# Kernel tuning notes

Hardware: AMD Instinct MI355X
Metric: run time of the kernel (lower is better)

Reference implementation:

```python
import jax, jax.numpy as jnp
import numpy as np

B, C, HID, A, K = 128, 2, 150, 8, 30
GRID = 49           # input maze size (forward crops to 49x49)
HP = GRID + 2       # 51: spatial size after kernel=3, padding=2 convs
KS = 3              # value-iteration kernel size


def conv(x, w, b=None, pad=1):
    y = jax.lax.conv_general_dilated(
        x, w, (1, 1), [(pad, pad), (pad, pad)],
        dimension_numbers=('NCHW', 'OIHW', 'NCHW'))
    if b is not None:
        y = y + b[None, :, None, None]
    return y


def unfold9(v):
    # v: [B,1,HP,HP] -> [B,9,HP,HP], 3x3 patches, padding=1 (matches F.unfold)
    vp = jnp.pad(v[:, 0], ((0, 0), (1, 1), (1, 1)))
    return jnp.stack([vp[:, i:i + HP, j:j + HP]
                      for i in range(KS) for j in range(KS)], axis=1)


def setup_inputs() -> dict:
    key = jax.random.key(0)
    ks = jax.random.split(key, 13)
    s = 0.05
    return {
        'grid': (jax.random.uniform(ks[0], (B, C, GRID, GRID)) < 0.3).astype(jnp.float32),
        'x_coord': jax.random.randint(ks[1], (B,), 0, GRID - 2),
        'y_coord': jax.random.randint(ks[2], (B,), 0, GRID - 2),
        'h1_w': jax.random.normal(ks[3], (HID, C, 3, 3)) * s,
        'h1_b': jax.random.normal(ks[4], (HID,)) * s,
        'h2_w': jax.random.normal(ks[5], (HID, HID, 3, 3)) * s,
        'h2_b': jax.random.normal(ks[6], (HID,)) * s,
        'r_w': jax.random.normal(ks[7], (1, HID, 3, 3)) * s,
        't_w': jax.random.normal(ks[8], (A * KS * KS, HID, 3, 3)) * s,
        'a1_w': jax.random.normal(ks[9], (HID, A)) * s,
        'a1_b': jax.random.normal(ks[10], (HID,)) * s,
        'a2_w': jax.random.normal(ks[11], (A, HID)) * s,
        'a2_b': jax.random.normal(ks[12], (A,)) * s,
    }


def reference(grid, x_coord, y_coord, h1_w, h1_b, h2_w, h2_b, r_w, t_w,
              a1_w, a1_b, a2_w, a2_b):
    # hidden feature extractor (padding=1, keeps 49x49)
    h = jax.nn.relu(conv(grid, h1_w, h1_b, pad=1))
    h = jax.nn.relu(conv(h, h2_w, h2_b, pad=1))
    # reward & dynamic transitions (kernel=3, padding=2 -> 51x51)
    reward = conv(h, r_w, None, pad=2)                 # [B,1,51,51]
    trans = conv(h, t_w, None, pad=2)                  # [B,A*9,51,51]
    # softmax over the 9-element kernel dim (loop-invariant in the original)
    sT = jax.nn.softmax(trans.reshape(B, A, KS * KS, HP, HP), axis=2)

    def step(carry, _):
        v, _ = carry
        patches = unfold9(v)                           # [B,9,51,51]
        q = jnp.einsum('bakhw,bkhw->bahw', sT, patches) + reward
        v_new = jnp.max(q, axis=1, keepdims=True)      # [B,1,51,51]
        return (v_new, q), None

    q0 = jnp.zeros((B, A, HP, HP), grid.dtype)
    (v, q_last), _ = jax.lax.scan(step, (jnp.zeros_like(reward), q0),
                                  None, length=K)

    # per-pixel action MLP on cropped q from the LAST iteration
    q_c = q_last[:, :, :GRID, :GRID]                   # [B,A,49,49]
    mid = jax.nn.relu(jnp.einsum('bahw,ca->bchw', q_c, a1_w)
                      + a1_b[None, :, None, None])
    logits = (jnp.einsum('bchw,ac->bahw', mid, a2_w)
              + a2_b[None, :, None, None])             # [B,A,49,49]
    return logits
```

## Files before the change

kernel.cpp:

```cpp
#include <hip/hip_runtime.h>
#include <hip/hip_bf16.h>
#include <stdint.h>

constexpr int NB   = 128;
constexpr int NC   = 2;
constexpr int NH   = 150;
constexpr int NA   = 8;
constexpr int KIT  = 30;
constexpr int GN   = 49;
constexpr int HPN  = 51;
constexpr int NP   = HPN * HPN;
constexpr int RTC  = 73;
constexpr int CIP  = 160;

typedef short v8bf __attribute__((ext_vector_type(8)));
typedef float v4f  __attribute__((ext_vector_type(4)));

__device__ __forceinline__ float bf_lo(uint32_t u){ return __uint_as_float(u << 16); }
__device__ __forceinline__ float bf_hi(uint32_t u){ return __uint_as_float(u & 0xffff0000u); }

__device__ __forceinline__ uint16_t f2bf(float f) {
    uint32_t u = __float_as_uint(f);
    uint32_t lsb = (u >> 16) & 1u;
    u += 0x7fffu + lsb;
    return (uint16_t)(u >> 16);
}

__device__ __forceinline__ float ld_f(const void* p, size_t i, int isbf) {
    if (isbf) {
        uint32_t b = ((const uint16_t*)p)[i];
        return __uint_as_float(b << 16);
    }
    return ((const float*)p)[i];
}
__device__ __forceinline__ uint16_t ld_bf_bits(const void* p, size_t i, int isbf) {
    if (isbf) return ((const uint16_t*)p)[i];
    return f2bf(((const float*)p)[i]);
}

__global__ void detect_kernel(const uint16_t* __restrict__ w, int* __restrict__ flag)
{
    int i = threadIdx.x;
    uint32_t bits = w[2 * i];
    float f = __uint_as_float(bits << 16);
    float a = fabsf(f);
    bool ok = (a >= 1e-10f && a <= 1e5f);
    unsigned long long m = __ballot(ok);
    if (i == 0) flag[0] = (__popcll(m) >= 48) ? 1 : 0;
}

__global__ void prep_kernel(const void* __restrict__ g,
                            const void* __restrict__ w1,
                            const void* __restrict__ b1,
                            const void* __restrict__ w2,
                            const void* __restrict__ b2,
                            const void* __restrict__ rw,
                            const void* __restrict__ tw,
                            const void* __restrict__ a1w,
                            const void* __restrict__ a1b,
                            const void* __restrict__ a2w,
                            const void* __restrict__ a2b,
                            const int* __restrict__ flag,
                            uint16_t* __restrict__ grid_cl,
                            float* __restrict__ wT1, float* __restrict__ bias1,
                            uint16_t* __restrict__ w2t, float* __restrict__ bias2,
                            uint16_t* __restrict__ wrt,
                            float* __restrict__ wA1, float* __restrict__ bA1,
                            float* __restrict__ wA2, float* __restrict__ bA2)
{
    constexpr int N_GRID = NB * GN * GN * NC;
    constexpr int N_WT1  = 9 * NC * NH;
    constexpr int N_B1   = NH;
    constexpr int N_W2T  = 9 * 5 * CIP * 32;
    constexpr int N_B2   = CIP;
    constexpr int N_WRT  = 9 * 5 * 80 * 32;
    constexpr int N_A1W  = NH * NA;
    constexpr int N_A1B  = NH;
    constexpr int N_A2W  = NA * NH;
    constexpr int N_A2B  = NA;

    int isbf = flag[0];
    int i = blockIdx.x * blockDim.x + threadIdx.x;
    if (i < N_GRID) {
        int c = i & 1; int s = (i >> 1) % (GN*GN); int b = i / (GN*GN*2);
        grid_cl[i] = ld_bf_bits(g, (size_t)(b*NC + c)*(GN*GN) + s, isbf);
        return;
    }
    i -= N_GRID;
    if (i < N_WT1) {
        int co = i % NH; int r = i / NH; int ci = r & 1; int k = r >> 1;
        wT1[i] = ld_f(w1, (size_t)co*(NC*9) + ci*9 + k, isbf);
        return;
    }
    i -= N_WT1;
    if (i < N_B1) { bias1[i] = ld_f(b1, i, isbf); return; }
    i -= N_B1;
    if (i < N_W2T) {
        int c  = i % 32;
        int co = (i / 32) % CIP;
        int kc = (i / (32*CIP)) % 5;
        int tap = i / (32*CIP*5);
        int ci = kc*32 + c;
        uint16_t v = 0;
        if (co < NH && ci < NH)
            v = f2bf(ld_f(w2, ((size_t)co*NH + ci)*9 + tap, isbf));
        w2t[i] = v;
        return;
    }
    i -= N_W2T;
    if (i < N_B2) { bias2[i] = (i < NH) ? ld_f(b2, i, isbf) : 0.f; return; }
    i -= N_B2;
    if (i < N_WRT) {
        int c  = i % 32;
        int co = (i / 32) % 80;
        int kc = (i / 2560) % 5;
        int tap = i / 12800;
        int ci = kc*32 + c;
        uint16_t v = 0;
        if (ci < NH) {
            if (co == 0)        v = f2bf(ld_f(rw, (size_t)ci*9 + tap, isbf));
            else if (co <= 72)  v = f2bf(ld_f(tw, ((size_t)(co-1)*NH + ci)*9 + tap, isbf));
        }
        wrt[i] = v;
        return;
    }
    i -= N_WRT;
    if (i < N_A1W) { wA1[i] = ld_f(a1w, i, isbf); return; }
    i -= N_A1W;
    if (i < N_A1B) { bA1[i] = ld_f(a1b, i, isbf); return; }
    i -= N_A1B;
    if (i < N_A2W) { wA2[i] = ld_f(a2w, i, isbf); return; }
    i -= N_A2W;
    if (i < N_A2B) { bA2[i] = ld_f(a2b, i, isbf); return; }
}

__global__ __launch_bounds__(192)
void conv1_cl(const uint16_t* __restrict__ in,
              const float* __restrict__ wT,
              const float* __restrict__ bias,
              uint16_t* __restrict__ out)
{
    constexpr int H = GN, XG = 13;
    int bid = blockIdx.x;
    int xg = bid % XG;
    int y  = (bid / XG) % H;
    int b  = bid / (XG * H);
    int x0 = xg * 4;
    int co = threadIdx.x;

    if (co >= NH) {
        if (co < CIP) {
            #pragma unroll
            for (int xi = 0; xi < 4; ++xi) {
                int x = x0 + xi;
                if (x < H) out[((size_t)(b*H + y)*H + x)*CIP + co] = 0;
            }
        }
        return;
    }

    float bv = bias[co];
    float acc[4] = {bv, bv, bv, bv};

    for (int ky = 0; ky < 3; ++ky) {
        int yy = y + ky - 1;
        if (yy < 0 || yy >= H) continue;
        const uint16_t* rowp = in + (size_t)(b * H + yy) * H * NC;
        #pragma unroll
        for (int kx = 0; kx < 3; ++kx) {
            const float* wp = wT + ((ky*3 + kx) * NC) * NH + co;
            float w0 = wp[0];
            float w1 = wp[NH];
            #pragma unroll
            for (int xi = 0; xi < 4; ++xi) {
                int xx = x0 + xi + kx - 1;
                if (xx < 0 || xx >= H) continue;
                uint32_t u = *(const uint32_t*)(rowp + (size_t)xx * NC);
                acc[xi] += bf_lo(u)*w0 + bf_hi(u)*w1;
            }
        }
    }
    #pragma unroll
    for (int xi = 0; xi < 4; ++xi) {
        int x = x0 + xi;
        if (x < H) out[((size_t)(b*H + y)*H + x)*CIP + co] = f2bf(fmaxf(acc[xi], 0.f));
    }
}

template<int CO_T, int CO_S, int PAD, int OH, bool RELU, bool OBF>
__global__ __launch_bounds__(192)
void conv_mfma(const uint16_t* __restrict__ in,
               const uint16_t* __restrict__ wt,
               const float* __restrict__ bias,
               void* __restrict__ outv)
{
    constexpr int H = GN;
    constexpr int NSUB = CO_S / 16;
    constexpr int CS = CO_T / CO_S;
    constexpr int AS = 168;
    constexpr int NST = 45;
    static_assert(NSUB * 16 == CO_S && CS * CO_S == CO_T, "");

    __shared__ __align__(16) uint16_t shA[8 * 18 * AS];

    int bid = blockIdx.x;
    int cs = 0;
    if (CS > 1) { cs = bid % CS; bid /= CS; }
    int xg = bid & 3;
    int rg = (bid >> 2) % 9;
    int b  = bid / 36;
    int y0 = rg * 6, x0 = xg * 16;
    int co0 = cs * CO_S;
    int t = threadIdx.x;
    int w = t >> 6, l = t & 63;
    int lo16 = l & 15, q4 = l >> 4;

    for (int q = t; q < 8*18*20; q += 192) {
        int ci8 = q % 20;
        int c   = (q / 20) % 18;
        int r   = q / 360;
        int yy = y0 + r - PAD, xx = x0 + c - PAD;
        uint4 v = make_uint4(0u, 0u, 0u, 0u);
        if (yy >= 0 && yy < H && xx >= 0 && xx < H)
            v = *(const uint4*)(in + ((size_t)(b*H + yy)*H + xx)*CIP + ci8*8);
        *(uint4*)(&shA[(r*18 + c)*AS + ci8*8]) = v;
    }
    __syncthreads();

    const uint16_t* wbase = wt + (size_t)co0*32 + lo16*32 + q4*8;

    v4f acc[2][NSUB];
    #pragma unroll
    for (int si = 0; si < 2; ++si)
        #pragma unroll
        for (int n = 0; n < NSUB; ++n)
            acc[si][n] = (v4f){0.f, 0.f, 0.f, 0.f};

    auto loadB = [&](int s, v8bf* bf) {
        const uint16_t* p = wbase + (size_t)s * (CO_T*32);
        #pragma unroll
        for (int n = 0; n < NSUB; ++n)
            bf[n] = *(const v8bf*)(p + n*512);
    };
    auto loadA = [&](int s, v8bf* af) {
        int tap = s / 5, kc = s % 5;
        int ky = tap / 3, kx = tap % 3;
        const uint16_t* base = &shA[((2*w + ky)*18 + lo16 + kx)*AS + kc*32 + q4*8];
        af[0] = *(const v8bf*)(base);
        af[1] = *(const v8bf*)(base + 18*AS);
    };
    auto compute = [&](v8bf* af, v8bf* bf) {
        #pragma unroll
        for (int n = 0; n < NSUB; ++n) {
            acc[0][n] = __builtin_amdgcn_mfma_f32_16x16x32_bf16(af[0], bf[n], acc[0][n], 0, 0, 0);
            acc[1][n] = __builtin_amdgcn_mfma_f32_16x16x32_bf16(af[1], bf[n], acc[1][n], 0, 0, 0);
        }
    };

    v8bf bf0[NSUB], bf1[NSUB], af0[2], af1[2];
    loadB(0, bf0); loadA(0, af0);
    for (int s = 0; s < NST - 1; s += 2) {
        loadB(s + 1, bf1); loadA(s + 1, af1);
        compute(af0, bf0);
        if (s + 2 < NST) { loadB(s + 2, bf0); loadA(s + 2, af0); }
        compute(af1, bf1);
    }
    compute(af0, bf0);

    #pragma unroll
    for (int si = 0; si < 2; ++si) {
        int y = y0 + 2*w + si;
        if (y >= OH) continue;
        #pragma unroll
        for (int n = 0; n < NSUB; ++n) {
            int co = co0 + n*16 + lo16;
            float bv = bias ? bias[co] : 0.f;
            #pragma unroll
            for (int r = 0; r < 4; ++r) {
                int x = x0 + q4*4 + r;
                if (x >= OH) continue;
                float v = acc[si][n][r] + bv;
                if (RELU) v = fmaxf(v, 0.f);
                if (OBF) {
                    ((uint16_t*)outv)[((size_t)(b*OH + y)*OH + x)*CIP + co] = f2bf(v);
                } else {
                    if (co < RTC)
                        ((float*)outv)[((size_t)(b*OH + y)*OH + x)*RTC + co] = v;
                }
            }
        }
    }
}

__global__ void softmax_pack_kernel(const float* __restrict__ rt,
                                    uint32_t* __restrict__ sTu,
                                    float* __restrict__ rewb)
{
    int idx = blockIdx.x * blockDim.x + threadIdx.x;
    constexpr int TOT = NB * NP;
    if (idx >= TOT) return;
    const float* tp = rt + (size_t)idx * RTC;
    rewb[idx] = tp[0];
    uint32_t words[36];
    #pragma unroll
    for (int a = 0; a < NA; ++a) {
        const float* s = tp + 1 + a * 9;
        float v[9];
        float m = -1e30f;
        #pragma unroll
        for (int k = 0; k < 9; ++k) { v[k] = s[k]; m = fmaxf(m, v[k]); }
        float sum = 0.f;
        #pragma unroll
        for (int k = 0; k < 9; ++k) { v[k] = expf(v[k] - m); sum += v[k]; }
        float sc = 65535.f / sum;
        #pragma unroll
        for (int k = 0; k < 9; ++k) {
            int gi = a * 9 + k;
            uint32_t u = (uint32_t)__float2uint_rn(v[k] * sc);
            if (gi & 1) words[gi >> 1] |= (u << 16);
            else        words[gi >> 1] = u;
        }
    }
    uint32_t* op = sTu + (size_t)idx * 36;
    #pragma unroll
    for (int j = 0; j < 9; ++j)
        *(uint4*)(op + 4*j) = make_uint4(words[4*j], words[4*j+1], words[4*j+2], words[4*j+3]);
}

__device__ __forceinline__ void vi_pair(const uint32_t* d, const float* pat,
                                        float r, float& qE, float& qO)
{
    float qe = 0.f, qo = 0.f;
    qe = fmaf((float)(d[0] & 0xffffu), pat[0], qe);
    qe = fmaf((float)(d[0] >> 16),     pat[1], qe);
    qe = fmaf((float)(d[1] & 0xffffu), pat[2], qe);
    qe = fmaf((float)(d[1] >> 16),     pat[3], qe);
    qe = fmaf((float)(d[2] & 0xffffu), pat[4], qe);
    qe = fmaf((float)(d[2] >> 16),     pat[5], qe);
    qe = fmaf((float)(d[3] & 0xffffu), pat[6], qe);
    qe = fmaf((float)(d[3] >> 16),     pat[7], qe);
    qe = fmaf((float)(d[4] & 0xffffu), pat[8], qe);
    qo = fmaf((float)(d[4] >> 16),     pat[0], qo);
    qo = fmaf((float)(d[5] & 0xffffu), pat[1], qo);
    qo = fmaf((float)(d[5] >> 16),     pat[2], qo);
    qo = fmaf((float)(d[6] & 0xffffu), pat[3], qo);
    qo = fmaf((float)(d[6] >> 16),     pat[4], qo);
    qo = fmaf((float)(d[7] & 0xffffu), pat[5], qo);
    qo = fmaf((float)(d[7] >> 16),     pat[6], qo);
    qo = fmaf((float)(d[8] & 0xffffu), pat[7], qo);
    qo = fmaf((float)(d[8] >> 16),     pat[8], qo);
    constexpr float inv = 1.f / 65535.f;
    qE = fmaf(qe, inv, r);
    qO = fmaf(qo, inv, r);
}

__global__ __launch_bounds__(1024, 1)
void vi_kernel(const uint32_t* __restrict__ sTu, const float* __restrict__ rewb,
               float* __restrict__ qout)
{
    __shared__ float vb[2][53*53];
    __shared__ float rew[NP];
    int b = blockIdx.x, t = threadIdx.x;
    for (int i = t; i < 53*53; i += 1024) { vb[0][i] = 0.f; vb[1][i] = 0.f; }
    const uint32_t* sb = sTu + (size_t)b * NP * 36;
    for (int i = t; i < NP; i += 1024) rew[i] = rewb[(size_t)b * NP + i];

    int p0 = t, p1 = t + 1024, p2 = t + 2048;
    uint32_t s0[36], s1[36];
    {
        const uint4* a0 = (const uint4*)(sb + (size_t)p0 * 36);
        const uint4* a1 = (const uint4*)(sb + (size_t)p1 * 36);
        #pragma unroll
        for (int j = 0; j < 9; ++j) {
            uint4 v = a0[j];
            s0[4*j+0]=v.x; s0[4*j+1]=v.y; s0[4*j+2]=v.z; s0[4*j+3]=v.w;
            uint4 u = a1[j];
            s1[4*j+0]=u.x; s1[4*j+1]=u.y; s1[4*j+2]=u.z; s1[4*j+3]=u.w;
        }
    }
    __syncthreads();

    float* qb = qout + (size_t)b * NP * NA;
    int cur = 0;
    for (int it = 0; it < KIT; ++it) {
        bool last = (it == KIT - 1);
        const float* vc = vb[cur];
        float* vn = vb[cur ^ 1];
        {
            int y = p0 / HPN, x = p0 % HPN;
            float pat[9];
            #pragma unroll
            for (int dy = 0; dy < 3; ++dy)
                #pragma unroll
                for (int dx = 0; dx < 3; ++dx)
                    pat[dy*3+dx] = vc[(y+dy)*53 + x+dx];
            float r = rew[p0];
            float best = -3.4e38f;
            #pragma unroll
            for (int ap = 0; ap < 4; ++ap) {
                float qE, qO;
                vi_pair(s0 + ap*9, pat, r, qE, qO);
                best = fmaxf(best, fmaxf(qE, qO));
                if (last) {
                    qb[(size_t)p0*NA + 2*ap]     = qE;
                    qb[(size_t)p0*NA + 2*ap + 1] = qO;
                }
            }
            vn[(y+1)*53 + x+1] = best;
        }
        {
            int y = p1 / HPN, x = p1 % HPN;
            float pat[9];
            #pragma unroll
            for (int dy = 0; dy < 3; ++dy)
                #pragma unroll
                for (int dx = 0; dx < 3; ++dx)
                    pat[dy*3+dx] = vc[(y+dy)*53 + x+dx];
            float r = rew[p1];
            float best = -3.4e38f;
            #pragma unroll
            for (int ap = 0; ap < 4; ++ap) {
                float qE, qO;
                vi_pair(s1 + ap*9, pat, r, qE, qO);
                best = fmaxf(best, fmaxf(qE, qO));
                if (last) {
                    qb[(size_t)p1*NA + 2*ap]     = qE;
                    qb[(size_t)p1*NA + 2*ap + 1] = qO;
                }
            }
            vn[(y+1)*53 + x+1] = best;
        }
        if (t < NP - 2048) {
            int y = p2 / HPN, x = p2 % HPN;
            float pat[9];
            #pragma unroll
            for (int dy = 0; dy < 3; ++dy)
                #pragma unroll
                for (int dx = 0; dx < 3; ++dx)
                    pat[dy*3+dx] = vc[(y+dy)*53 + x+dx];
            float r = rew[p2];
            float best = -3.4e38f;
            const uint32_t* gp = sb + (size_t)p2 * 36;
            #pragma unroll
            for (int ap = 0; ap < 4; ++ap) {
                uint32_t d[9];
                #pragma unroll
                for (int j = 0; j < 9; ++j) d[j] = gp[ap*9 + j];
                float qE, qO;
                vi_pair(d, pat, r, qE, qO);
                best = fmaxf(best, fmaxf(qE, qO));
                if (last) {
                    qb[(size_t)p2*NA + 2*ap]     = qE;
                    qb[(size_t)p2*NA + 2*ap + 1] = qO;
                }
            }
            vn[(y+1)*53 + x+1] = best;
        }
        __syncthreads();
        cur ^= 1;
    }
}

__global__ void head_kernel(const float* __restrict__ q,
                            const float* __restrict__ wA1,
                            const float* __restrict__ bA1,
                            const float* __restrict__ wA2,
                            const float* __restrict__ bA2,
                            const int* __restrict__ flag,
                            void* __restrict__ out)
{
    __shared__ float w1[NH*NA], sb1[NH], w2[NA*NH], sb2[NA];
    int t = threadIdx.x;
    for (int i = t; i < NH*NA; i += 256) w1[i] = wA1[i];
    for (int i = t; i < NH;    i += 256) sb1[i] = bA1[i];
    for (int i = t; i < NA*NH; i += 256) w2[i] = wA2[i];
    if (t < NA) sb2[t] = bA2[t];
    __syncthreads();

    int isbf = flag[0];
    int idx = blockIdx.x * 256 + t;
    constexpr int TOT = NB * GN * GN;
    if (idx >= TOT) return;
    int x = idx % GN, y = (idx / GN) % GN, b = idx / (GN*GN);
    const float* qp = q + ((size_t)(b*HPN + y)*HPN + x) * NA;
    float qv[NA];
    #pragma unroll
    for (int a = 0; a < NA; ++a) qv[a] = qp[a];
    float lg[NA];
    #pragma unroll
    for (int a = 0; a < NA; ++a) lg[a] = sb2[a];
    for (int c = 0; c < NH; ++c) {
        float m = sb1[c];
        #pragma unroll
        for (int a = 0; a < NA; ++a) m += qv[a] * w1[c*NA + a];
        m = fmaxf(m, 0.f);
        #pragma unroll
        for (int a = 0; a < NA; ++a) lg[a] += m * w2[a*NH + c];
    }
    #pragma unroll
    for (int a = 0; a < NA; ++a) {
        size_t oi = ((size_t)(b*NA + a)*GN + y)*GN + x;
        float r = lg[a];
        if (isbf) ((uint16_t*)out)[oi] = f2bf(r);
        else      ((float*)out)[oi] = r;
    }
}

extern "C" void kernel_launch(void* const* d_in, const int* in_sizes, int n_in,
                              void* d_out, int out_size, void* d_ws, size_t ws_size,
                              hipStream_t stream)
{
    const void* g   = d_in[0];
    const void* h1w = d_in[3];
    const void* h1b = d_in[4];
    const void* h2w = d_in[5];
    const void* h2b = d_in[6];
    const void* rw  = d_in[7];
    const void* tw  = d_in[8];
    const void* a1w = d_in[9];
    const void* a1b = d_in[10];
    const void* a2w = d_in[11];
    const void* a2b = d_in[12];

    char* ws = (char*)d_ws;
    size_t off = 0;
    auto take = [&](size_t bytes) { size_t r = off; off = (off + bytes + 255) & ~(size_t)255; return r; };

    constexpr size_t N_GRID_CL = (size_t)NB*GN*GN*NC;
    constexpr size_t N_WT1  = 9*NC*NH;
    constexpr size_t N_B1   = NH;
    constexpr size_t N_W2T  = 9*5*CIP*32;
    constexpr size_t N_B2   = CIP;
    constexpr size_t N_WRT  = 9*5*80*32;
    constexpr size_t N_A1W  = NH*NA;
    constexpr size_t N_A1B  = NH;
    constexpr size_t N_A2W  = NA*NH;
    constexpr size_t N_A2B  = NA;
    constexpr size_t N_H    = (size_t)NB*GN*GN*CIP;
    constexpr size_t N_RT   = (size_t)NB*NP*RTC;
    constexpr size_t N_Q    = (size_t)NB*NP*NA;
    constexpr size_t N_STU  = (size_t)NB*NP*36;
    constexpr size_t N_REWB = (size_t)NB*NP;

    size_t off_flag   = take(4);
    size_t off_gridcl = take(N_GRID_CL * 2);
    size_t off_wT1    = take(N_WT1 * 4);
    size_t off_b1     = take(N_B1 * 4);
    size_t off_w2t    = take(N_W2T * 2);
    size_t off_b2     = take(N_B2 * 4);
    size_t off_wrt    = take(N_WRT * 2);
    size_t off_wA1    = take(N_A1W * 4);
    size_t off_bA1    = take(N_A1B * 4);
    size_t off_wA2    = take(N_A2W * 4);
    size_t off_bA2    = take(N_A2B * 4);
    size_t off_q      = take(N_Q * 4);
    size_t szA = (N_RT * 4 > N_H * 2) ? N_RT * 4 : N_H * 2;
    size_t off_A      = take(szA);
    size_t szB = N_H * 2;
    size_t szB2 = ((N_STU * 4 + 255) & ~(size_t)255) + N_REWB * 4;
    if (szB2 > szB) szB = szB2;
    size_t off_B      = take(szB);

    int*      flag    = (int*)(ws + off_flag);
    uint16_t* grid_cl = (uint16_t*)(ws + off_gridcl);
    float*    wT1     = (float*)(ws + off_wT1);
    float*    bias1   = (float*)(ws + off_b1);
    uint16_t* w2t     = (uint16_t*)(ws + off_w2t);
    float*    bias2   = (float*)(ws + off_b2);
    uint16_t* wrt     = (uint16_t*)(ws + off_wrt);
    float*    wA1     = (float*)(ws + off_wA1);
    float*    bA1     = (float*)(ws + off_bA1);
    float*    wA2     = (float*)(ws + off_wA2);
    float*    bA2     = (float*)(ws + off_bA2);
    float*    qbuf    = (float*)(ws + off_q);
    uint16_t* h1      = (uint16_t*)(ws + off_A);
    float*    rt      = (float*)(ws + off_A);
    uint16_t* h2      = (uint16_t*)(ws + off_B);
    uint32_t* sTu     = (uint32_t*)(ws + off_B);
    float*    rewb    = (float*)(ws + off_B + ((N_STU * 4 + 255) & ~(size_t)255));

    detect_kernel<<<1, 64, 0, stream>>>((const uint16_t*)h2w, flag);
    {
        int total = (int)(N_GRID_CL + N_WT1 + N_B1 + N_W2T + N_B2 + N_WRT
                          + N_A1W + N_A1B + N_A2W + N_A2B);
        prep_kernel<<<(total + 255)/256, 256, 0, stream>>>(
            g, h1w, h1b, h2w, h2b, rw, tw, a1w, a1b, a2w, a2b, flag,
            grid_cl, wT1, bias1, w2t, bias2, wrt, wA1, bA1, wA2, bA2);
    }
    conv1_cl<<<NB*GN*13, 192, 0, stream>>>(grid_cl, wT1, bias1, h1);
    conv_mfma<CIP, 80, 1, GN, true, true>
        <<<NB*36*2, 192, 0, stream>>>(h1, w2t, bias2, (void*)h2);
    conv_mfma<80, 80, 2, HPN, false, false>
        <<<NB*36, 192, 0, stream>>>(h2, wrt, nullptr, (void*)rt);
    softmax_pack_kernel<<<(NB*NP + 255)/256, 256, 0, stream>>>(rt, sTu, rewb);
    vi_kernel<<<NB, 1024, 0, stream>>>(sTu, rewb, qbuf);
    head_kernel<<<(NB*GN*GN + 255)/256, 256, 0, stream>>>(qbuf, wA1, bA1, wA2, bA2, flag,
                                                          d_out);
}
```

Baseline: 1.281 ms.

## Split conv halo staging into two channel phases to shrink LDS footprint

The MFMA conv kernel now stages the input halo in two channel chunks (3 then 2 of the 5 k-chunks), computing each phase before reloading shared memory. This cuts LDS per block from 168 to 104 stride, which should allow more resident blocks per CU. The cost is extra barriers, a serialized second global load without overlap, and shorter MFMA pipelines per phase.

```diff
diff --git a/kernel.cpp b/kernel.cpp
--- a/kernel.cpp
+++ b/kernel.cpp
@@ -197,11 +197,10 @@
     constexpr int H = GN;
     constexpr int NSUB = CO_S / 16;
     constexpr int CS = CO_T / CO_S;
-    constexpr int AS = 168;
-    constexpr int NST = 45;
+    constexpr int ASP = 104;
     static_assert(NSUB * 16 == CO_S && CS * CO_S == CO_T, "");
 
-    __shared__ __align__(16) uint16_t shA[8 * 18 * AS];
+    __shared__ __align__(16) uint16_t shA[8 * 18 * ASP];
 
     int bid = blockIdx.x;
     int cs = 0;
@@ -215,17 +214,20 @@
     int w = t >> 6, l = t & 63;
     int lo16 = l & 15, q4 = l >> 4;
 
-    for (int q = t; q < 8*18*20; q += 192) {
-        int ci8 = q % 20;
-        int c   = (q / 20) % 18;
-        int r   = q / 360;
-        int yy = y0 + r - PAD, xx = x0 + c - PAD;
-        uint4 v = make_uint4(0u, 0u, 0u, 0u);
-        if (yy >= 0 && yy < H && xx >= 0 && xx < H)
-            v = *(const uint4*)(in + ((size_t)(b*H + yy)*H + xx)*CIP + ci8*8);
-        *(uint4*)(&shA[(r*18 + c)*AS + ci8*8]) = v;
-    }
-    __syncthreads();
+    auto stageHalo = [&](int kcBase, int nkc) {
+        int nch = nkc * 4;
+        int total = 8 * 18 * nch;
+        for (int q = t; q < total; q += 192) {
+            int ci8 = q % nch;
+            int c   = (q / nch) % 18;
+            int r   = q / (nch * 18);
+            int yy = y0 + r - PAD, xx = x0 + c - PAD;
+            uint4 v = make_uint4(0u, 0u, 0u, 0u);
+            if (yy >= 0 && yy < H && xx >= 0 && xx < H)
+                v = *(const uint4*)(in + ((size_t)(b*H + yy)*H + xx)*CIP + kcBase*32 + ci8*8);
+            *(uint4*)(&shA[(r*18 + c)*ASP + ci8*8]) = v;
+        }
+    };
 
     const uint16_t* wbase = wt + (size_t)co0*32 + lo16*32 + q4*8;
 
@@ -236,18 +238,18 @@
         for (int n = 0; n < NSUB; ++n)
             acc[si][n] = (v4f){0.f, 0.f, 0.f, 0.f};
 
-    auto loadB = [&](int s, v8bf* bf) {
-        const uint16_t* p = wbase + (size_t)s * (CO_T*32);
+    auto loadB = [&](int sg, v8bf* bf) {
+        const uint16_t* p = wbase + (size_t)sg * (CO_T*32);
         #pragma unroll
         for (int n = 0; n < NSUB; ++n)
             bf[n] = *(const v8bf*)(p + n*512);
     };
-    auto loadA = [&](int s, v8bf* af) {
-        int tap = s / 5, kc = s % 5;
+    auto loadA = [&](int sg, int kcBase, v8bf* af) {
+        int tap = sg / 5, kc = sg % 5;
         int ky = tap / 3, kx = tap % 3;
-        const uint16_t* base = &shA[((2*w + ky)*18 + lo16 + kx)*AS + kc*32 + q4*8];
+        const uint16_t* base = &shA[((2*w + ky)*18 + lo16 + kx)*ASP + (kc - kcBase)*32 + q4*8];
         af[0] = *(const v8bf*)(base);
-        af[1] = *(const v8bf*)(base + 18*AS);
+        af[1] = *(const v8bf*)(base + 18*ASP);
     };
     auto compute = [&](v8bf* af, v8bf* bf) {
         #pragma unroll
@@ -257,15 +259,27 @@
         }
     };
 
-    v8bf bf0[NSUB], bf1[NSUB], af0[2], af1[2];
-    loadB(0, bf0); loadA(0, af0);
-    for (int s = 0; s < NST - 1; s += 2) {
-        loadB(s + 1, bf1); loadA(s + 1, af1);
-        compute(af0, bf0);
-        if (s + 2 < NST) { loadB(s + 2, bf0); loadA(s + 2, af0); }
-        compute(af1, bf1);
-    }
-    compute(af0, bf0);
+    auto phase = [&](int kcBase, int nkc) {
+        int nst = 9 * nkc;
+        auto sg = [&](int i){ int tap = i / nkc, kco = i % nkc; return tap*5 + kcBase + kco; };
+        v8bf bf0[NSUB], bf1[NSUB], af0[2], af1[2];
+        loadB(sg(0), bf0); loadA(sg(0), kcBase, af0);
+        for (int i = 0; i < nst - 1; i += 2) {
+            loadB(sg(i+1), bf1); loadA(sg(i+1), kcBase, af1);
+            compute(af0, bf0);
+            if (i + 2 < nst) { loadB(sg(i+2), bf0); loadA(sg(i+2), kcBase, af0); }
+            compute(af1, bf1);
+        }
+        if (nst & 1) compute(af0, bf0);
+    };
+
+    stageHalo(0, 3);
+    __syncthreads();
+    phase(0, 3);
+    __syncthreads();
+    stageHalo(3, 2);
+    __syncthreads();
+    phase(3, 2);
 
     #pragma unroll
     for (int si = 0; si < 2; ++si) {
```

Result: no change. 1.265 ms (-1.2%).
